# Optimization experiments

Hardware: AMD Instinct MI355X
Metric: run time of the kernel (lower is better)

The kernel has to match this reference:

```python
import jax, jax.numpy as jnp
import numpy as np

B_SZ, L_SEQ, D_MODEL, D_STATE = 4, 2048, 1024, 16


def setup_inputs() -> dict:
    key = jax.random.key(0)
    ks = jax.random.split(key, 6)
    x = jax.random.normal(ks[0], (B_SZ, L_SEQ, D_MODEL), jnp.float32)
    # HiPPO-inspired init: A_log = log(arange(1..n)).clamp(min=-7), broadcast over channels
    A_log = jnp.clip(jnp.log(jnp.arange(1, D_STATE + 1, dtype=jnp.float32)), -7.0, None)
    A_log = jnp.broadcast_to(A_log[None, :], (D_MODEL, D_STATE)).astype(jnp.float32)
    B_param = 0.02 * jax.random.normal(ks[1], (D_MODEL, D_STATE), jnp.float32)
    C_param = 0.02 * jax.random.normal(ks[2], (D_MODEL, D_STATE), jnp.float32)
    log_dt = 0.01 * jax.random.normal(ks[3], (D_MODEL,), jnp.float32) - 4.0
    in_w = jax.random.normal(ks[4], (2 * D_MODEL, D_MODEL), jnp.float32) / np.sqrt(D_MODEL).astype(np.float32)
    in_b = jnp.zeros((2 * D_MODEL,), jnp.float32)
    out_w = jax.random.normal(ks[5], (D_MODEL, D_MODEL), jnp.float32) / np.sqrt(D_MODEL).astype(np.float32)
    out_b = jnp.zeros((D_MODEL,), jnp.float32)
    ln_g = jnp.ones((D_MODEL,), jnp.float32)
    ln_b = jnp.zeros((D_MODEL,), jnp.float32)
    return {"x": x, "A_log": A_log, "B_param": B_param, "C_param": C_param,
            "log_dt": log_dt, "in_w": in_w, "in_b": in_b, "out_w": out_w,
            "out_b": out_b, "ln_g": ln_g, "ln_b": ln_b}


def _ssm_scan(u, A_log, B_param, C_param, log_dt):
    # u: (B, L, D). Builds kernel h[t,d] = sum_n A_bar[d,n]^t * C[d,n]*B[d,n]*dt[d]
    # and applies a causal depthwise convolution (via FFT; same math as conv1d).
    L = u.shape[1]
    dt = jnp.clip(jnp.exp(log_dt), 1e-4, 1.0)                      # (D,)
    A_bar = jnp.exp(-jnp.exp(A_log) * dt[:, None])                 # ZOH discretisation (D,N)
    A_bar = jnp.clip(A_bar, 1e-8, 1.0 - 1e-8)
    log_A = jnp.log(A_bar)                                         # (D,N)
    t_idx = jnp.arange(L, dtype=jnp.float32)                       # (L,)
    A_powers = jnp.exp(t_idx[:, None, None] * log_A[None, :, :])   # (L,D,N)
    cb_dt = C_param * B_param * dt[:, None]                        # (D,N)
    kernel = jnp.einsum('ldn,dn->ld', A_powers, cb_dt)             # (L,D)
    # causal conv: y[b,t,d] = sum_{tau<=t} kernel[tau,d] * u[b,t-tau,d]
    n_fft = 2 * L
    Kf = jnp.fft.rfft(kernel, n=n_fft, axis=0)                     # (n_fft/2+1, D)
    Uf = jnp.fft.rfft(u, n=n_fft, axis=1)                          # (B, n_fft/2+1, D)
    y = jnp.fft.irfft(Uf * Kf[None], n=n_fft, axis=1)[:, :L]       # (B,L,D)
    return y.astype(u.dtype)


def reference(x, A_log, B_param, C_param, log_dt, in_w, in_b, out_w, out_b, ln_g, ln_b):
    x = x.astype(jnp.float32)
    residual = x
    # LayerNorm (eps=1e-5)
    mu = jnp.mean(x, axis=-1, keepdims=True)
    var = jnp.mean(jnp.square(x - mu), axis=-1, keepdims=True)
    xn = (x - mu) * jax.lax.rsqrt(var + 1e-5) * ln_g + ln_b
    xz = xn @ in_w.T + in_b                                        # (B,L,2D)
    x_proj, z = xz[..., :D_MODEL], xz[..., D_MODEL:]
    z = jax.nn.silu(z)
    y = _ssm_scan(x_proj, A_log, B_param, C_param, log_dt)
    y = y * z
    y = y @ out_w.T + out_b
    # dropout is identity in eval mode
    return jnp.clip(y + residual, -10.0, 10.0)
```

## Files before the change

kernel.cpp:

```cpp
#include <hip/hip_runtime.h>
#include <hip/hip_bf16.h>

#define D_MODEL 1024
#define D_STATE 16
#define L_SEQ 2048
#define B_SZ 4
#define M_ROWS (B_SZ * L_SEQ)
#define N_CHUNK 32
#define C_LEN 64

typedef __attribute__((ext_vector_type(8))) short short8;
typedef __attribute__((ext_vector_type(4))) float f32x4;

#define SBAR()  asm volatile("s_barrier" ::: "memory")
#define GATE(N) asm volatile("s_waitcnt vmcnt(" #N ") lgkmcnt(0)\n\ts_barrier" ::: "memory")

typedef const unsigned short __attribute__((address_space(1))) gas_us;
typedef unsigned short __attribute__((address_space(3))) las_us;
static __device__ __forceinline__ void gload16(const unsigned short* g, unsigned short* l) {
    __builtin_amdgcn_global_load_lds((gas_us*)g, (las_us*)l, 16, 0, 0);
}

static __device__ __forceinline__ unsigned short f2bf(float f) {
    unsigned int u = __float_as_uint(f);
    unsigned int r = (u + 0x7FFFu + ((u >> 16) & 1u)) >> 16;
    return (unsigned short)r;
}
static __device__ __forceinline__ float bf2f(unsigned short u) {
    return __uint_as_float(((unsigned int)u) << 16);
}

__global__ void conv_bf16_kernel(const float* __restrict__ src,
                                 unsigned short* __restrict__ dst, int n4) {
    int i = blockIdx.x * blockDim.x + threadIdx.x;
    if (i < n4) {
        float4 v = ((const float4*)src)[i];
        ushort4 o;
        o.x = f2bf(v.x); o.y = f2bf(v.y); o.z = f2bf(v.z); o.w = f2bf(v.w);
        ((ushort4*)dst)[i] = o;
    }
}

__global__ __launch_bounds__(256) void ln_kernel(const float* __restrict__ x,
                                                 const float* __restrict__ g,
                                                 const float* __restrict__ b,
                                                 unsigned short* __restrict__ xn) {
    int row = blockIdx.x;
    int t = threadIdx.x;
    const float4* xr = (const float4*)(x + (size_t)row * D_MODEL);
    float4 v = xr[t];
    float s  = v.x + v.y + v.z + v.w;
    float ss = v.x * v.x + v.y * v.y + v.z * v.z + v.w * v.w;
    #pragma unroll
    for (int o = 32; o > 0; o >>= 1) {
        s  += __shfl_down(s,  o);
        ss += __shfl_down(ss, o);
    }
    __shared__ float sbuf[8];
    int wid = t >> 6;
    if ((t & 63) == 0) { sbuf[wid] = s; sbuf[4 + wid] = ss; }
    __syncthreads();
    float S  = sbuf[0] + sbuf[1] + sbuf[2] + sbuf[3];
    float SS = sbuf[4] + sbuf[5] + sbuf[6] + sbuf[7];
    float mu  = S * (1.0f / D_MODEL);
    float var = SS * (1.0f / D_MODEL) - mu * mu;
    float inv = rsqrtf(var + 1e-5f);
    float4 gv = ((const float4*)g)[t];
    float4 bv = ((const float4*)b)[t];
    ushort4 o;
    o.x = f2bf((v.x - mu) * inv * gv.x + bv.x);
    o.y = f2bf((v.y - mu) * inv * gv.y + bv.y);
    o.z = f2bf((v.z - mu) * inv * gv.z + bv.z);
    o.w = f2bf((v.w - mu) * inv * gv.w + bv.w);
    ((ushort4*)(xn + (size_t)row * D_MODEL))[t] = o;
}

#define MFMA16(ACC, I0, AV, BV) { \
    _Pragma("unroll") for (int i_ = 0; i_ < 4; ++i_) { \
        _Pragma("unroll") for (int jf_ = 0; jf_ < 4; ++jf_) \
            ACC[(I0) + i_][jf_] = __builtin_amdgcn_mfma_f32_16x16x32_bf16( \
                AV[i_], BV[jf_], ACC[(I0) + i_][jf_], 0, 0, 0); } }

#define STAGE1A(J) { size_t ko_ = (size_t)(J) * 32; int so_ = ((J) & 3) * 16384; \
    gload16(pA0 + ko_, dA0 + so_); gload16(pA1 + ko_, dA1 + so_); }
#define STAGE1B(J) { size_t ko_ = (size_t)(J) * 32; int so_ = ((J) & 3) * 16384; \
    gload16(pB0 + ko_, dB0 + so_); gload16(pB1 + ko_, dB1 + so_); }

#define G1_TILE(J, DOSTAGE, TRAIL) { \
    const int slot_ = (J) & 3; \
    const char* rA_ = ldsA_rd + slot_ * 32768; \
    const char* rB_ = ldsB_rd + slot_ * 32768; \
    short8 av[4], bv[4]; \
    _Pragma("unroll") for (int j_ = 0; j_ < 4; ++j_) bv[j_] = *(const short8*)(rB_ + j_ * 1024); \
    _Pragma("unroll") for (int i_ = 0; i_ < 4; ++i_) av[i_] = *(const short8*)(rA_ + i_ * 1024); \
    if (DOSTAGE) { STAGE1A((J) + 3); } \
    SBAR(); \
    __builtin_amdgcn_s_setprio(1); \
    MFMA16(acc, 0, av, bv); \
    __builtin_amdgcn_s_setprio(0); \
    SBAR(); \
    _Pragma("unroll") for (int i_ = 0; i_ < 4; ++i_) av[i_] = *(const short8*)(rA_ + 4096 + i_ * 1024); \
    if (DOSTAGE) { STAGE1B((J) + 3); } \
    SBAR(); \
    __builtin_amdgcn_s_setprio(1); \
    MFMA16(acc, 4, av, bv); \
    __builtin_amdgcn_s_setprio(0); \
    TRAIL; \
}

__global__ __launch_bounds__(512, 2) void gemm1_kernel(const unsigned short* __restrict__ A,
                                                       const unsigned short* __restrict__ Bt,
                                                       const float* __restrict__ bias,
                                                       unsigned short* __restrict__ u_bf,
                                                       unsigned short* __restrict__ zs) {
    __shared__ __align__(16) unsigned short lds[4][2][8192];
    const int K = D_MODEL;

    int t = threadIdx.x;
    int lane = t & 63;
    int wave = t >> 6;
    int wm = wave >> 2;
    int wn = wave & 3;

    int bid = blockIdx.x;
    int swz = (bid & 7) * 32 + (bid >> 3);
    int m0 = (swz >> 3) * 256;
    int n0 = (swz & 7) * 256;

    int srow = lane >> 2;
    int sk = ((lane & 3) * 8) ^ ((lane & 32) >> 1);
    const unsigned short* pA0 = A  + (size_t)(m0 + wave * 16 + srow) * K + sk;
    const unsigned short* pA1 = pA0 + (size_t)128 * K;
    const unsigned short* pB0 = Bt + (size_t)(n0 + wave * 16 + srow) * K + sk;
    const unsigned short* pB1 = pB0 + (size_t)128 * K;

    unsigned short* dA0 = &lds[0][0][wave * 512];
    unsigned short* dA1 = &lds[0][0][(8 + wave) * 512];
    unsigned short* dB0 = &lds[0][1][wave * 512];
    unsigned short* dB1 = &lds[0][1][(8 + wave) * 512];

    int off_base = (lane & 15) * 64 + (((lane >> 4) * 16) ^ ((lane & 8) * 4));
    const char* ldsA_rd = (const char*)(&lds[0][0][0]) + wm * 8192 + off_base;
    const char* ldsB_rd = (const char*)(&lds[0][1][0]) + wn * 4096 + off_base;

    f32x4 acc[8][4] = {};

    STAGE1A(0); STAGE1B(0); STAGE1A(1); STAGE1B(1); STAGE1A(2); STAGE1B(2);
    GATE(8);

    #pragma unroll 1
    for (int j = 0; j < 29; ++j) { G1_TILE(j, true, GATE(8)); }
    G1_TILE(29, false, GATE(4));
    G1_TILE(30, false, GATE(0));
    G1_TILE(31, false, (void)0);

    int col = lane & 15;
    int quad = lane >> 4;
    #pragma unroll
    for (int jf = 0; jf < 4; ++jf) {
        int n = n0 + wn * 64 + jf * 16 + col;
        float bs = bias[n];
        bool isU = (n < D_MODEL);
        #pragma unroll
        for (int i = 0; i < 8; ++i) {
            #pragma unroll
            for (int r = 0; r < 4; ++r) {
                int m = m0 + wm * 128 + i * 16 + quad * 4 + r;
                float v = acc[i][jf][r] + bs;
                if (isU) {
                    u_bf[(size_t)m * D_MODEL + n] = f2bf(v);
                } else {
                    float sv = v / (1.0f + __expf(-v));
                    zs[(size_t)m * D_MODEL + (n - D_MODEL)] = f2bf(sv);
                }
            }
        }
    }
}

#define STAGE2(J) { size_t ko_ = (size_t)(J) * 32; int so_ = ((J) & 3) * 12288; \
    gload16(pA0 + ko_, dA + so_); gload16(pB0 + ko_, dB0 + so_); gload16(pB1 + ko_, dB1 + so_); }

#define G2_TILE(J, DOSTAGE, TRAIL) { \
    const int slot_ = (J) & 3; \
    const char* rA_ = ldsA_rd + slot_ * 24576; \
    const char* rB_ = ldsB_rd + slot_ * 24576; \
    short8 av[4], bv[4]; \
    _Pragma("unroll") for (int i_ = 0; i_ < 4; ++i_) av[i_] = *(const short8*)(rA_ + i_ * 1024); \
    _Pragma("unroll") for (int j_ = 0; j_ < 4; ++j_) bv[j_] = *(const short8*)(rB_ + j_ * 1024); \
    if (DOSTAGE) { STAGE2((J) + 3); } \
    SBAR(); \
    __builtin_amdgcn_s_setprio(1); \
    MFMA16(acc, 0, av, bv); \
    __builtin_amdgcn_s_setprio(0); \
    TRAIL; \
}

__global__ __launch_bounds__(512, 2) void gemm2_kernel(const unsigned short* __restrict__ A,
                                                       const unsigned short* __restrict__ Bt,
                                                       const float* __restrict__ bias,
                                                       float* __restrict__ out_f,
                                                       const float* __restrict__ resid) {
    __shared__ __align__(16) unsigned short lds[4][12288];
    const int K = D_MODEL;

    int t = threadIdx.x;
    int lane = t & 63;
    int wave = t >> 6;
    int wm = wave >> 2;
    int wn = wave & 3;

    int bid = blockIdx.x;
    int swz = (bid & 7) * 32 + (bid >> 3);
    int m0 = (swz >> 2) * 128;
    int n0 = (swz & 3) * 256;

    int srow = lane >> 2;
    int sk = ((lane & 3) * 8) ^ ((lane & 32) >> 1);
    const unsigned short* pA0 = A  + (size_t)(m0 + wave * 16 + srow) * K + sk;
    const unsigned short* pB0 = Bt + (size_t)(n0 + wave * 16 + srow) * K + sk;
    const unsigned short* pB1 = pB0 + (size_t)128 * K;

    unsigned short* dA  = &lds[0][wave * 512];
    unsigned short* dB0 = &lds[0][4096 + wave * 512];
    unsigned short* dB1 = &lds[0][8192 + wave * 512];

    int off_base = (lane & 15) * 64 + (((lane >> 4) * 16) ^ ((lane & 8) * 4));
    const char* ldsA_rd = (const char*)(&lds[0][0]) + wm * 4096 + off_base;
    const char* ldsB_rd = (const char*)(&lds[0][0]) + 8192 + wn * 4096 + off_base;

    f32x4 acc[4][4] = {};

    STAGE2(0); STAGE2(1); STAGE2(2);
    GATE(6);

    #pragma unroll 1
    for (int j = 0; j < 29; ++j) { G2_TILE(j, true, GATE(6)); }
    G2_TILE(29, false, GATE(3));
    G2_TILE(30, false, GATE(0));
    G2_TILE(31, false, (void)0);

    int col = lane & 15;
    int quad = lane >> 4;
    #pragma unroll
    for (int jf = 0; jf < 4; ++jf) {
        int n = n0 + wn * 64 + jf * 16 + col;
        float bs = bias[n];
        #pragma unroll
        for (int i = 0; i < 4; ++i) {
            #pragma unroll
            for (int r = 0; r < 4; ++r) {
                int m = m0 + wm * 64 + i * 16 + quad * 4 + r;
                float y = acc[i][jf][r] + bs + resid[(size_t)m * D_MODEL + n];
                y = fminf(10.0f, fmaxf(-10.0f, y));
                out_f[(size_t)m * D_MODEL + n] = y;
            }
        }
    }
}

static __device__ __forceinline__ void load_params(const float* __restrict__ A_log,
                                                   const float* __restrict__ log_dt,
                                                   int d, float* ab, float& dt_out) {
    float dt = fminf(1.0f, fmaxf(1e-4f, __expf(log_dt[d])));
    #pragma unroll
    for (int n = 0; n < D_STATE; n++) {
        float a = __expf(-__expf(A_log[d * D_STATE + n]) * dt);
        ab[n] = fminf(1.0f - 1e-8f, fmaxf(1e-8f, a));
    }
    dt_out = dt;
}

__global__ __launch_bounds__(256) void scan1_kernel(const unsigned short* __restrict__ u,
                                                    const float* __restrict__ A_log,
                                                    const float* __restrict__ log_dt,
                                                    float* __restrict__ s_local) {
    int gid = blockIdx.x * 256 + threadIdx.x;
    int d = gid & (D_MODEL - 1);
    int c = (gid >> 10) & (N_CHUNK - 1);
    int b = gid >> 15;

    float ab[D_STATE], dt;
    load_params(A_log, log_dt, d, ab, dt);

    float s[D_STATE];
    #pragma unroll
    for (int n = 0; n < D_STATE; n++) s[n] = 0.0f;

    const unsigned short* up = u + ((size_t)(b * L_SEQ + c * C_LEN)) * D_MODEL + d;
    for (int t = 0; t < C_LEN; t++) {
        float uv = bf2f(up[(size_t)t * D_MODEL]);
        #pragma unroll
        for (int n = 0; n < D_STATE; n++) s[n] = fmaf(ab[n], s[n], uv);
    }
    float* sl = s_local + ((size_t)(b * N_CHUNK + c) * D_STATE) * D_MODEL + d;
    #pragma unroll
    for (int n = 0; n < D_STATE; n++) sl[(size_t)n * D_MODEL] = s[n];
}

__global__ __launch_bounds__(256) void scan_combine_kernel(const float* __restrict__ s_local,
                                                           const float* __restrict__ A_log,
                                                           const float* __restrict__ log_dt,
                                                           float* __restrict__ s_init) {
    int gid = blockIdx.x * 256 + threadIdx.x;
    int d = gid & (D_MODEL - 1);
    int n = (gid >> 10) & (D_STATE - 1);
    int b = gid >> 14;

    float dt = fminf(1.0f, fmaxf(1e-4f, __expf(log_dt[d])));
    float a = __expf(-__expf(A_log[d * D_STATE + n]) * dt);
    a = fminf(1.0f - 1e-8f, fmaxf(1e-8f, a));
    float aP = a;
    #pragma unroll
    for (int q = 0; q < 6; q++) aP = aP * aP;

    float s = 0.0f;
    size_t stride_c = (size_t)D_STATE * D_MODEL;
    const float* sl = s_local + ((size_t)b * N_CHUNK * D_STATE + n) * D_MODEL + d;
    float* si = s_init + ((size_t)b * N_CHUNK * D_STATE + n) * D_MODEL + d;
    si[0] = 0.0f;
    for (int c = 1; c < N_CHUNK; c++) {
        s = fmaf(aP, s, sl[(size_t)(c - 1) * stride_c]);
        si[(size_t)c * stride_c] = s;
    }
}

__global__ __launch_bounds__(256) void scan2_kernel(const unsigned short* __restrict__ u,
                                                    const unsigned short* __restrict__ zs,
                                                    const float* __restrict__ A_log,
                                                    const float* __restrict__ Bp,
                                                    const float* __restrict__ Cp,
                                                    const float* __restrict__ log_dt,
                                                    const float* __restrict__ s_init,
                                                    unsigned short* __restrict__ yz) {
    int gid = blockIdx.x * 256 + threadIdx.x;
    int d = gid & (D_MODEL - 1);
    int c = (gid >> 10) & (N_CHUNK - 1);
    int b = gid >> 15;

    float ab[D_STATE], dt;
    load_params(A_log, log_dt, d, ab, dt);
    float cb[D_STATE];
    #pragma unroll
    for (int n = 0; n < D_STATE; n++)
        cb[n] = Cp[d * D_STATE + n] * Bp[d * D_STATE + n] * dt;

    float s[D_STATE];
    const float* si = s_init + ((size_t)(b * N_CHUNK + c) * D_STATE) * D_MODEL + d;
    #pragma unroll
    for (int n = 0; n < D_STATE; n++) s[n] = si[(size_t)n * D_MODEL];

    size_t m0 = (size_t)(b * L_SEQ + c * C_LEN);
    const unsigned short* up = u + m0 * D_MODEL + d;
    const unsigned short* zp = zs + m0 * D_MODEL + d;
    unsigned short* yp = yz + m0 * D_MODEL + d;

    for (int t = 0; t < C_LEN; t++) {
        float uv = bf2f(up[(size_t)t * D_MODEL]);
        #pragma unroll
        for (int n = 0; n < D_STATE; n++) s[n] = fmaf(ab[n], s[n], uv);
        float y = 0.0f;
        #pragma unroll
        for (int n = 0; n < D_STATE; n++) y = fmaf(cb[n], s[n], y);
        float zv = bf2f(zp[(size_t)t * D_MODEL]);
        yp[(size_t)t * D_MODEL] = f2bf(y * zv);
    }
}

extern "C" void kernel_launch(void* const* d_in, const int* in_sizes, int n_in,
                              void* d_out, int out_size, void* d_ws, size_t ws_size,
                              hipStream_t stream) {
    const float* x       = (const float*)d_in[0];
    const float* A_log   = (const float*)d_in[1];
    const float* B_param = (const float*)d_in[2];
    const float* C_param = (const float*)d_in[3];
    const float* log_dt  = (const float*)d_in[4];
    const float* in_w    = (const float*)d_in[5];
    const float* in_b    = (const float*)d_in[6];
    const float* out_w   = (const float*)d_in[7];
    const float* out_b   = (const float*)d_in[8];
    const float* ln_g    = (const float*)d_in[9];
    const float* ln_b    = (const float*)d_in[10];
    float* out = (float*)d_out;

    char* ws = (char*)d_ws;
    size_t off = 0;
    unsigned short* xn = (unsigned short*)(ws + off); off += (size_t)M_ROWS * D_MODEL * 2;
    unsigned short* w1 = (unsigned short*)(ws + off); off += (size_t)2 * D_MODEL * D_MODEL * 2;
    unsigned short* u  = (unsigned short*)(ws + off); off += (size_t)M_ROWS * D_MODEL * 2;
    unsigned short* zs = (unsigned short*)(ws + off); off += (size_t)M_ROWS * D_MODEL * 2;
    unsigned short* yz = (unsigned short*)(ws + off); off += (size_t)M_ROWS * D_MODEL * 2;
    unsigned short* w2 = (unsigned short*)(ws + off); off += (size_t)D_MODEL * D_MODEL * 2;
    float* s_local = (float*)(ws + off); off += (size_t)B_SZ * N_CHUNK * D_STATE * D_MODEL * 4;
    float* s_init  = (float*)(ws + off); off += (size_t)B_SZ * N_CHUNK * D_STATE * D_MODEL * 4;

    {
        int n4 = 2 * D_MODEL * D_MODEL / 4;
        conv_bf16_kernel<<<(n4 + 255) / 256, 256, 0, stream>>>(in_w, w1, n4);
    }
    {
        int n4 = D_MODEL * D_MODEL / 4;
        conv_bf16_kernel<<<(n4 + 255) / 256, 256, 0, stream>>>(out_w, w2, n4);
    }

    ln_kernel<<<M_ROWS, 256, 0, stream>>>(x, ln_g, ln_b, xn);

    gemm1_kernel<<<256, 512, 0, stream>>>(xn, w1, in_b, u, zs);

    scan1_kernel<<<(B_SZ * N_CHUNK * D_MODEL) / 256, 256, 0, stream>>>(u, A_log, log_dt, s_local);
    scan_combine_kernel<<<(B_SZ * D_STATE * D_MODEL) / 256, 256, 0, stream>>>(s_local, A_log, log_dt, s_init);
    scan2_kernel<<<(B_SZ * N_CHUNK * D_MODEL) / 256, 256, 0, stream>>>(
        u, zs, A_log, B_param, C_param, log_dt, s_init, yz);

    gemm2_kernel<<<256, 512, 0, stream>>>(yz, w2, out_b, out, x);
}
```

Measured before the change: 214.3 us.

## Fuse LN and weight casts into one prep kernel; restructure gemm1 tile loop

Merges the two weight bf16-conversion launches and the LayerNorm launch into a single prep kernel, removing two kernel launches. In gemm1 it loads all eight A fragments at once and issues all 32 MFMAs per k-step with a single barrier, dropping the mid-tile barrier pair. The occupancy hint goes from 2 to 1 block per SM, which raises register pressure. Both GEMM epilogues are reordered to hoist bias loads and the u/z branch out of the inner loops.

```diff
diff --git a/kernel.cpp b/kernel.cpp
--- a/kernel.cpp
+++ b/kernel.cpp
@@ -30,90 +30,90 @@
     return __uint_as_float(((unsigned int)u) << 16);
 }
 
-__global__ void conv_bf16_kernel(const float* __restrict__ src,
-                                 unsigned short* __restrict__ dst, int n4) {
-    int i = blockIdx.x * blockDim.x + threadIdx.x;
-    if (i < n4) {
-        float4 v = ((const float4*)src)[i];
+__global__ __launch_bounds__(256) void prep_kernel(const float* __restrict__ x,
+                                                   const float* __restrict__ g,
+                                                   const float* __restrict__ b,
+                                                   unsigned short* __restrict__ xn,
+                                                   const float* __restrict__ in_w,
+                                                   unsigned short* __restrict__ w1,
+                                                   const float* __restrict__ out_w,
+                                                   unsigned short* __restrict__ w2) {
+    __shared__ float sbuf[8];
+    int bid = blockIdx.x;
+    int t = threadIdx.x;
+    if (bid < M_ROWS) {
+        int row = bid;
+        const float4* xr = (const float4*)(x + (size_t)row * D_MODEL);
+        float4 v = xr[t];
+        float s  = v.x + v.y + v.z + v.w;
+        float ss = v.x * v.x + v.y * v.y + v.z * v.z + v.w * v.w;
+        #pragma unroll
+        for (int o = 32; o > 0; o >>= 1) {
+            s  += __shfl_down(s,  o);
+            ss += __shfl_down(ss, o);
+        }
+        int wid = t >> 6;
+        if ((t & 63) == 0) { sbuf[wid] = s; sbuf[4 + wid] = ss; }
+        __syncthreads();
+        float S  = sbuf[0] + sbuf[1] + sbuf[2] + sbuf[3];
+        float SS = sbuf[4] + sbuf[5] + sbuf[6] + sbuf[7];
+        float mu  = S * (1.0f / D_MODEL);
+        float var = SS * (1.0f / D_MODEL) - mu * mu;
+        float inv = rsqrtf(var + 1e-5f);
+        float4 gv = ((const float4*)g)[t];
+        float4 bv = ((const float4*)b)[t];
+        ushort4 o;
+        o.x = f2bf((v.x - mu) * inv * gv.x + bv.x);
+        o.y = f2bf((v.y - mu) * inv * gv.y + bv.y);
+        o.z = f2bf((v.z - mu) * inv * gv.z + bv.z);
+        o.w = f2bf((v.w - mu) * inv * gv.w + bv.w);
+        ((ushort4*)(xn + (size_t)row * D_MODEL))[t] = o;
+    } else if (bid < M_ROWS + 2048) {
+        int i = (bid - M_ROWS) * 256 + t;
+        float4 v = ((const float4*)in_w)[i];
         ushort4 o;
         o.x = f2bf(v.x); o.y = f2bf(v.y); o.z = f2bf(v.z); o.w = f2bf(v.w);
-        ((ushort4*)dst)[i] = o;
-    }
-}
-
-__global__ __launch_bounds__(256) void ln_kernel(const float* __restrict__ x,
-                                                 const float* __restrict__ g,
-                                                 const float* __restrict__ b,
-                                                 unsigned short* __restrict__ xn) {
-    int row = blockIdx.x;
-    int t = threadIdx.x;
-    const float4* xr = (const float4*)(x + (size_t)row * D_MODEL);
-    float4 v = xr[t];
-    float s  = v.x + v.y + v.z + v.w;
-    float ss = v.x * v.x + v.y * v.y + v.z * v.z + v.w * v.w;
-    #pragma unroll
-    for (int o = 32; o > 0; o >>= 1) {
-        s  += __shfl_down(s,  o);
-        ss += __shfl_down(ss, o);
-    }
-    __shared__ float sbuf[8];
-    int wid = t >> 6;
-    if ((t & 63) == 0) { sbuf[wid] = s; sbuf[4 + wid] = ss; }
-    __syncthreads();
-    float S  = sbuf[0] + sbuf[1] + sbuf[2] + sbuf[3];
-    float SS = sbuf[4] + sbuf[5] + sbuf[6] + sbuf[7];
-    float mu  = S * (1.0f / D_MODEL);
-    float var = SS * (1.0f / D_MODEL) - mu * mu;
-    float inv = rsqrtf(var + 1e-5f);
-    float4 gv = ((const float4*)g)[t];
-    float4 bv = ((const float4*)b)[t];
-    ushort4 o;
-    o.x = f2bf((v.x - mu) * inv * gv.x + bv.x);
-    o.y = f2bf((v.y - mu) * inv * gv.y + bv.y);
-    o.z = f2bf((v.z - mu) * inv * gv.z + bv.z);
-    o.w = f2bf((v.w - mu) * inv * gv.w + bv.w);
-    ((ushort4*)(xn + (size_t)row * D_MODEL))[t] = o;
-}
-
-#define MFMA16(ACC, I0, AV, BV) { \
-    _Pragma("unroll") for (int i_ = 0; i_ < 4; ++i_) { \
+        ((ushort4*)w1)[i] = o;
+    } else {
+        int i = (bid - M_ROWS - 2048) * 256 + t;
+        float4 v = ((const float4*)out_w)[i];
+        ushort4 o;
+        o.x = f2bf(v.x); o.y = f2bf(v.y); o.z = f2bf(v.z); o.w = f2bf(v.w);
+        ((ushort4*)w2)[i] = o;
+    }
+}
+
+#define MFMA32(ACC, AV, BV) { \
+    _Pragma("unroll") for (int i_ = 0; i_ < 8; ++i_) { \
         _Pragma("unroll") for (int jf_ = 0; jf_ < 4; ++jf_) \
-            ACC[(I0) + i_][jf_] = __builtin_amdgcn_mfma_f32_16x16x32_bf16( \
-                AV[i_], BV[jf_], ACC[(I0) + i_][jf_], 0, 0, 0); } }
-
-#define STAGE1A(J) { size_t ko_ = (size_t)(J) * 32; int so_ = ((J) & 3) * 16384; \
-    gload16(pA0 + ko_, dA0 + so_); gload16(pA1 + ko_, dA1 + so_); }
-#define STAGE1B(J) { size_t ko_ = (size_t)(J) * 32; int so_ = ((J) & 3) * 16384; \
+            ACC[i_][jf_] = __builtin_amdgcn_mfma_f32_16x16x32_bf16( \
+                AV[i_], BV[jf_], ACC[i_][jf_], 0, 0, 0); } }
+
+#define STAGE1(J) { size_t ko_ = (size_t)(J) * 32; int so_ = ((J) & 3) * 16384; \
+    gload16(pA0 + ko_, dA0 + so_); gload16(pA1 + ko_, dA1 + so_); \
     gload16(pB0 + ko_, dB0 + so_); gload16(pB1 + ko_, dB1 + so_); }
 
 #define G1_TILE(J, DOSTAGE, TRAIL) { \
     const int slot_ = (J) & 3; \
     const char* rA_ = ldsA_rd + slot_ * 32768; \
     const char* rB_ = ldsB_rd + slot_ * 32768; \
-    short8 av[4], bv[4]; \
+    short8 av[8], bv[4]; \
+    _Pragma("unroll") for (int i_ = 0; i_ < 8; ++i_) av[i_] = *(const short8*)(rA_ + i_ * 1024); \
     _Pragma("unroll") for (int j_ = 0; j_ < 4; ++j_) bv[j_] = *(const short8*)(rB_ + j_ * 1024); \
-    _Pragma("unroll") for (int i_ = 0; i_ < 4; ++i_) av[i_] = *(const short8*)(rA_ + i_ * 1024); \
-    if (DOSTAGE) { STAGE1A((J) + 3); } \
+    if (DOSTAGE) { STAGE1((J) + 3); } \
     SBAR(); \
     __builtin_amdgcn_s_setprio(1); \
-    MFMA16(acc, 0, av, bv); \
-    __builtin_amdgcn_s_setprio(0); \
-    SBAR(); \
-    _Pragma("unroll") for (int i_ = 0; i_ < 4; ++i_) av[i_] = *(const short8*)(rA_ + 4096 + i_ * 1024); \
-    if (DOSTAGE) { STAGE1B((J) + 3); } \
-    SBAR(); \
-    __builtin_amdgcn_s_setprio(1); \
-    MFMA16(acc, 4, av, bv); \
+    MFMA32(acc, av, bv); \
     __builtin_amdgcn_s_setprio(0); \
     TRAIL; \
 }
 
-__global__ __launch_bounds__(512, 2) void gemm1_kernel(const unsigned short* __restrict__ A,
+__global__ __launch_bounds__(512, 1) void gemm1_kernel(const unsigned short* __restrict__ A,
                                                        const unsigned short* __restrict__ Bt,
                                                        const float* __restrict__ bias,
                                                        unsigned short* __restrict__ u_bf,
                                                        unsigned short* __restrict__ zs) {
-    __shared__ __align__(16) unsigned short lds[4][2][8192];
+    __shared__ __align__(16) unsigned short lds[4][16384];
     const int K = D_MODEL;
 
     int t = threadIdx.x;
@@ -134,18 +134,18 @@
     const unsigned short* pB0 = Bt + (size_t)(n0 + wave * 16 + srow) * K + sk;
     const unsigned short* pB1 = pB0 + (size_t)128 * K;
 
-    unsigned short* dA0 = &lds[0][0][wave * 512];
-    unsigned short* dA1 = &lds[0][0][(8 + wave) * 512];
-    unsigned short* dB0 = &lds[0][1][wave * 512];
-    unsigned short* dB1 = &lds[0][1][(8 + wave) * 512];
+    unsigned short* dA0 = &lds[0][wave * 512];
+    unsigned short* dA1 = &lds[0][4096 + wave * 512];
+    unsigned short* dB0 = &lds[0][8192 + wave * 512];
+    unsigned short* dB1 = &lds[0][12288 + wave * 512];
 
     int off_base = (lane & 15) * 64 + (((lane >> 4) * 16) ^ ((lane & 8) * 4));
-    const char* ldsA_rd = (const char*)(&lds[0][0][0]) + wm * 8192 + off_base;
-    const char* ldsB_rd = (const char*)(&lds[0][1][0]) + wn * 4096 + off_base;
+    const char* ldsA_rd = (const char*)(&lds[0][0]) + wm * 8192 + off_base;
+    const char* ldsB_rd = (const char*)(&lds[0][0]) + 16384 + wn * 4096 + off_base;
 
     f32x4 acc[8][4] = {};
 
-    STAGE1A(0); STAGE1B(0); STAGE1A(1); STAGE1B(1); STAGE1A(2); STAGE1B(2);
+    STAGE1(0); STAGE1(1); STAGE1(2);
     GATE(8);
 
     #pragma unroll 1
@@ -156,27 +156,33 @@
 
     int col = lane & 15;
     int quad = lane >> 4;
-    #pragma unroll
-    for (int jf = 0; jf < 4; ++jf) {
-        int n = n0 + wn * 64 + jf * 16 + col;
-        float bs = bias[n];
-        bool isU = (n < D_MODEL);
-        #pragma unroll
-        for (int i = 0; i < 8; ++i) {
+    float bs[4];
+    #pragma unroll
+    for (int jf = 0; jf < 4; ++jf) bs[jf] = bias[n0 + wn * 64 + jf * 16 + col];
+    bool isU = (n0 < D_MODEL);
+    int nbase = isU ? (n0 + wn * 64 + col) : (n0 - D_MODEL + wn * 64 + col);
+    unsigned short* obase = isU ? u_bf : zs;
+    #pragma unroll
+    for (int i = 0; i < 8; ++i) {
+        #pragma unroll
+        for (int r = 0; r < 4; ++r) {
+            int m = m0 + wm * 128 + i * 16 + quad * 4 + r;
+            unsigned short* orow = obase + (size_t)m * D_MODEL + nbase;
             #pragma unroll
-            for (int r = 0; r < 4; ++r) {
-                int m = m0 + wm * 128 + i * 16 + quad * 4 + r;
-                float v = acc[i][jf][r] + bs;
-                if (isU) {
-                    u_bf[(size_t)m * D_MODEL + n] = f2bf(v);
-                } else {
-                    float sv = v / (1.0f + __expf(-v));
-                    zs[(size_t)m * D_MODEL + (n - D_MODEL)] = f2bf(sv);
-                }
+            for (int jf = 0; jf < 4; ++jf) {
+                float v = acc[i][jf][r] + bs[jf];
+                if (!isU) v = v / (1.0f + __expf(-v));
+                orow[jf * 16] = f2bf(v);
             }
         }
     }
 }
+
+#define MFMA16(ACC, AV, BV) { \
+    _Pragma("unroll") for (int i_ = 0; i_ < 4; ++i_) { \
+        _Pragma("unroll") for (int jf_ = 0; jf_ < 4; ++jf_) \
+            ACC[i_][jf_] = __builtin_amdgcn_mfma_f32_16x16x32_bf16( \
+                AV[i_], BV[jf_], ACC[i_][jf_], 0, 0, 0); } }
 
 #define STAGE2(J) { size_t ko_ = (size_t)(J) * 32; int so_ = ((J) & 3) * 12288; \
     gload16(pA0 + ko_, dA + so_); gload16(pB0 + ko_, dB0 + so_); gload16(pB1 + ko_, dB1 + so_); }
@@ -191,7 +197,7 @@
     if (DOSTAGE) { STAGE2((J) + 3); } \
     SBAR(); \
     __builtin_amdgcn_s_setprio(1); \
-    MFMA16(acc, 0, av, bv); \
+    MFMA16(acc, av, bv); \
     __builtin_amdgcn_s_setprio(0); \
     TRAIL; \
 }
@@ -242,18 +248,21 @@
 
     int col = lane & 15;
     int quad = lane >> 4;
-    #pragma unroll
-    for (int jf = 0; jf < 4; ++jf) {
-        int n = n0 + wn * 64 + jf * 16 + col;
-        float bs = bias[n];
-        #pragma unroll
-        for (int i = 0; i < 4; ++i) {
+    float bs[4];
+    #pragma unroll
+    for (int jf = 0; jf < 4; ++jf) bs[jf] = bias[n0 + wn * 64 + jf * 16 + col];
+    #pragma unroll
+    for (int i = 0; i < 4; ++i) {
+        #pragma unroll
+        for (int r = 0; r < 4; ++r) {
+            int m = m0 + wm * 64 + i * 16 + quad * 4 + r;
+            const float* rrow = resid + (size_t)m * D_MODEL + n0 + wn * 64 + col;
+            float* orow = out_f + (size_t)m * D_MODEL + n0 + wn * 64 + col;
             #pragma unroll
-            for (int r = 0; r < 4; ++r) {
-                int m = m0 + wm * 64 + i * 16 + quad * 4 + r;
-                float y = acc[i][jf][r] + bs + resid[(size_t)m * D_MODEL + n];
+            for (int jf = 0; jf < 4; ++jf) {
+                float y = acc[i][jf][r] + bs[jf] + rrow[jf * 16];
                 y = fminf(10.0f, fmaxf(-10.0f, y));
-                out_f[(size_t)m * D_MODEL + n] = y;
+                orow[jf * 16] = y;
             }
         }
     }
@@ -394,16 +403,7 @@
     float* s_local = (float*)(ws + off); off += (size_t)B_SZ * N_CHUNK * D_STATE * D_MODEL * 4;
     float* s_init  = (float*)(ws + off); off += (size_t)B_SZ * N_CHUNK * D_STATE * D_MODEL * 4;
 
-    {
-        int n4 = 2 * D_MODEL * D_MODEL / 4;
-        conv_bf16_kernel<<<(n4 + 255) / 256, 256, 0, stream>>>(in_w, w1, n4);
-    }
-    {
-        int n4 = D_MODEL * D_MODEL / 4;
-        conv_bf16_kernel<<<(n4 + 255) / 256, 256, 0, stream>>>(out_w, w2, n4);
-    }
-
-    ln_kernel<<<M_ROWS, 256, 0, stream>>>(x, ln_g, ln_b, xn);
+    prep_kernel<<<M_ROWS + 2048 + 1024, 256, 0, stream>>>(x, ln_g, ln_b, xn, in_w, w1, out_w, w2);
 
     gemm1_kernel<<<256, 512, 0, stream>>>(xn, w1, in_b, u, zs);
 
```

Result: faster. 206.1 us (-3.8%).
